# Kernel tuning notes

Measured on AMD Instinct MI355X. Metric: run time of the kernel, lower is better.

The kernel has to match this reference:

```python
import jax, jax.numpy as jnp
import numpy as np

N, T, D, H = 256, 64, 1024, 1024


def setup_inputs() -> dict:
    key = jax.random.key(0)
    k1, k2, k3, k4, k5 = jax.random.split(key, 5)
    x = jax.random.normal(k1, (N, T, D), dtype=jnp.float32)
    A = jax.random.normal(k2, (N, H, 4, 4), dtype=jnp.float32)
    Wx = jax.random.normal(k3, (D, 4 * H), dtype=jnp.float32) / np.sqrt(D)
    Wh = jax.random.normal(k4, (H, 4 * H), dtype=jnp.float32) / np.sqrt(H)
    Wattn = jax.random.normal(k5, (H, 4 * H), dtype=jnp.float32) / np.sqrt(H)
    b = jnp.zeros((4 * H,), dtype=jnp.float32)
    return {"x": x, "A": A, "Wx": Wx, "Wh": Wh, "Wattn": Wattn, "b": b}


def reference(x, A, Wx, Wh, Wattn, b):
    n, t, d = x.shape
    h_dim = A.shape[1]
    L = A.shape[2] * A.shape[3]  # 16 spatial locations
    A_flat = A.reshape(n, h_dim, L)  # (N, H, 16)
    scale = 1.0 / (h_dim ** 0.5)
    h0 = A_flat.mean(axis=2)  # global mean-pooled feature, (N, H)
    c0 = h0

    def step(carry, xt):
        h, c = carry
        # scaled dot-product attention over 4x4 grid
        w = jax.nn.softmax(jnp.einsum('nh,nhl->nl', h, A_flat) * scale, axis=1)
        attn = jnp.einsum('nhl,nl->nh', A_flat, w)
        a = h @ Wh + xt @ Wx + attn @ Wattn + b  # (N, 4H)
        a_i, a_f, a_o, a_g = jnp.split(a, 4, axis=1)
        i = jax.nn.sigmoid(a_i)
        f = jax.nn.sigmoid(a_f)
        o = jax.nn.sigmoid(a_o)
        g = jnp.tanh(a_g)
        c_next = f * c + i * g
        h_next = o * jnp.tanh(c_next)
        return (h_next, c_next), h_next

    xs = jnp.swapaxes(x, 0, 1)  # (T, N, D)
    _, hs = jax.lax.scan(step, (h0, c0), xs)
    return jnp.swapaxes(hs, 0, 1)  # (N, T, H)
```

## Files before the change

kernel.cpp:

```cpp
#include <hip/hip_runtime.h>
#include <math.h>

#define NB 256
#define TT 64
#define DD 1024
#define HH 1024

typedef __attribute__((ext_vector_type(8))) short short8;
typedef __attribute__((ext_vector_type(4))) float floatx4;

__device__ inline unsigned short f2bf(float f) {
    unsigned int u = __builtin_bit_cast(unsigned int, f);
    u += 0x7fffu + ((u >> 16) & 1u);
    return (unsigned short)(u >> 16);
}
__device__ inline float bf2f(unsigned int h16) {
    unsigned int u = h16 << 16;
    return __builtin_bit_cast(float, u);
}

__device__ inline void async_copy16(const unsigned short* g, unsigned short* l) {
    __builtin_amdgcn_global_load_lds(
        (const __attribute__((address_space(1))) unsigned int*)(g),
        (__attribute__((address_space(3))) unsigned int*)(l), 16, 0, 0);
}

__global__ void k_convW(const float* __restrict__ Wh,
                        const float* __restrict__ Wattn,
                        const float* __restrict__ Wx,
                        unsigned short* __restrict__ Wsw) {
    int u = blockIdx.x * 256 + threadIdx.x;
    int tile = u >> 9;
    int nj = tile / 48, kc = tile % 48;
    int within = u & 511;
    int kq = within >> 6, cc = within & 63;
    int k = kc * 64 + kq * 8;
    int col = (cc >> 4) * 1024 + nj * 16 + (cc & 15);
    const float* src;
    if (k < 1024)       src = Wh    + (size_t)k * 4096 + col;
    else if (k < 2048)  src = Wattn + (size_t)(k - 1024) * 4096 + col;
    else                src = Wx    + (size_t)(k - 2048) * 4096 + col;
    unsigned int w[4];
#pragma unroll
    for (int j = 0; j < 4; ++j) {
        unsigned int lo = f2bf(src[(size_t)(2 * j) * 4096]);
        unsigned int hi = f2bf(src[(size_t)(2 * j + 1) * 4096]);
        w[j] = lo | (hi << 16);
    }
    ((uint4*)Wsw)[u] = make_uint4(w[0], w[1], w[2], w[3]);
}

__global__ void k_convX(const float* __restrict__ x, unsigned short* __restrict__ xF) {
    int u = blockIdx.x * 256 + threadIdx.x;
    int t = u >> 15;
    int kq = (u >> 8) & 127;
    int m = u & 255;
    const float* src = x + (size_t)m * (TT * DD) + t * DD + kq * 8;
    float4 v0 = ((const float4*)src)[0];
    float4 v1 = ((const float4*)src)[1];
    unsigned int w0 = f2bf(v0.x) | (f2bf(v0.y) << 16);
    unsigned int w1 = f2bf(v0.z) | (f2bf(v0.w) << 16);
    unsigned int w2 = f2bf(v1.x) | (f2bf(v1.y) << 16);
    unsigned int w3 = f2bf(v1.z) | (f2bf(v1.w) << 16);
    ((uint4*)xF)[u] = make_uint4(w0, w1, w2, w3);
}

__global__ void k_convA_init(const float* __restrict__ A,
                             unsigned short* __restrict__ Abf,
                             float* __restrict__ h0,
                             float* __restrict__ c) {
    int idx = blockIdx.x * 256 + threadIdx.x;
    const float4* ap = (const float4*)(A + (size_t)idx * 16);
    float4 v0 = ap[0], v1 = ap[1], v2 = ap[2], v3 = ap[3];
    float vs[16] = {v0.x, v0.y, v0.z, v0.w, v1.x, v1.y, v1.z, v1.w,
                    v2.x, v2.y, v2.z, v2.w, v3.x, v3.y, v3.z, v3.w};
    float s = 0.f;
    unsigned int w[8];
#pragma unroll
    for (int j = 0; j < 8; ++j) {
        s += vs[2 * j] + vs[2 * j + 1];
        w[j] = f2bf(vs[2 * j]) | (f2bf(vs[2 * j + 1]) << 16);
    }
    ((uint4*)Abf)[idx * 2]     = make_uint4(w[0], w[1], w[2], w[3]);
    ((uint4*)Abf)[idx * 2 + 1] = make_uint4(w[4], w[5], w[6], w[7]);
    s *= (1.f / 16.f);
    h0[idx] = s;
    c[idx] = s;
}

__global__ __launch_bounds__(256) void k_attn(
    const unsigned short* __restrict__ Abf,
    const float* __restrict__ hprev, int hstride,
    unsigned short* __restrict__ lhsF) {
    const int n = blockIdx.x;
    const int tid = threadIdx.x;
    const int lane = tid & 63, wave = tid >> 6;

    float4 hv = *(const float4*)(hprev + (size_t)n * hstride + tid * 4);
    const uint4* ar = (const uint4*)(Abf + ((size_t)n * 1024 + tid * 4) * 16);

    float a[4][16];
#pragma unroll
    for (int r = 0; r < 4; ++r) {
        uint4 p0 = ar[r * 2], p1 = ar[r * 2 + 1];
        unsigned int ws[8] = {p0.x, p0.y, p0.z, p0.w, p1.x, p1.y, p1.z, p1.w};
#pragma unroll
        for (int j = 0; j < 8; ++j) {
            a[r][2 * j]     = bf2f(ws[j] & 0xffffu);
            a[r][2 * j + 1] = bf2f(ws[j] >> 16);
        }
    }
    float hvv[4] = {hv.x, hv.y, hv.z, hv.w};
    float s[16];
#pragma unroll
    for (int l = 0; l < 16; ++l) {
        float t = 0.f;
#pragma unroll
        for (int r = 0; r < 4; ++r) t += hvv[r] * a[r][l];
        s[l] = t;
    }

#pragma unroll
    for (int off = 32; off > 0; off >>= 1) {
#pragma unroll
        for (int l = 0; l < 16; ++l) s[l] += __shfl_xor(s[l], off, 64);
    }
    __shared__ float wred[4 * 16];
    if (lane == 0) {
#pragma unroll
        for (int l = 0; l < 16; ++l) wred[wave * 16 + l] = s[l];
    }
    __syncthreads();

    const float scale = 0.03125f;
    float sv[16];
#pragma unroll
    for (int l = 0; l < 16; ++l)
        sv[l] = (wred[l] + wred[16 + l] + wred[32 + l] + wred[48 + l]) * scale;
    float mx = sv[0];
#pragma unroll
    for (int l = 1; l < 16; ++l) mx = fmaxf(mx, sv[l]);
    float e[16], sum = 0.f;
#pragma unroll
    for (int l = 0; l < 16; ++l) { e[l] = __expf(sv[l] - mx); sum += e[l]; }
    float inv = 1.f / sum;
#pragma unroll
    for (int l = 0; l < 16; ++l) e[l] *= inv;

    unsigned short hb[4], ab[4];
#pragma unroll
    for (int r = 0; r < 4; ++r) {
        float acc = 0.f;
#pragma unroll
        for (int l = 0; l < 16; ++l) acc += a[r][l] * e[l];
        ab[r] = f2bf(acc);
        hb[r] = f2bf(hvv[r]);
    }
    unsigned int hw0 = (unsigned int)hb[0] | ((unsigned int)hb[1] << 16);
    unsigned int hw1 = (unsigned int)hb[2] | ((unsigned int)hb[3] << 16);
    unsigned int aw0 = (unsigned int)ab[0] | ((unsigned int)ab[1] << 16);
    unsigned int aw1 = (unsigned int)ab[2] | ((unsigned int)ab[3] << 16);
    size_t hu = ((size_t)(tid >> 1) * 256 + n) * 8 + (size_t)(tid & 1) * 4;
    size_t au = ((size_t)(128 + (tid >> 1)) * 256 + n) * 8 + (size_t)(tid & 1) * 4;
    *(uint2*)(lhsF + hu) = make_uint2(hw0, hw1);
    *(uint2*)(lhsF + au) = make_uint2(aw0, aw1);
}

__global__ __launch_bounds__(256) void k_step(
    const unsigned short* __restrict__ lhsF,
    const unsigned short* __restrict__ xFt,
    const unsigned short* __restrict__ Wsw,
    const float* __restrict__ b,
    float* __restrict__ c,
    float* __restrict__ out_t) {
    const int nj = blockIdx.x, mi = blockIdx.y;
    const int tid = threadIdx.x;
    const int lane = tid & 63, wave = tid >> 6;
    const int wm = wave & 1, wn = wave >> 1;
    const int l15 = lane & 15, quad = lane >> 4;
    const int waveBase = tid & ~63;

    __shared__ __align__(16) unsigned short lds[4 * 8192];

    floatx4 acc[2][2];
#pragma unroll
    for (int mt = 0; mt < 2; ++mt)
#pragma unroll
        for (int nt = 0; nt < 2; ++nt) acc[mt][nt] = (floatx4)0.f;

    const unsigned short* wTile = Wsw + (size_t)nj * (48 * 512 * 8);

    auto stage = [&](int kc, int buf) {
        unsigned short* la = lds + (size_t)buf * 8192;
        unsigned short* lb = la + 4096;
        const unsigned short* as_ = (kc < 32)
            ? lhsF + ((size_t)(kc * 8) * 256 + (size_t)mi * 64) * 8
            : xFt + ((size_t)((kc - 32) * 8) * 256 + (size_t)mi * 64) * 8;
#pragma unroll
        for (int i = 0; i < 2; ++i) {
            int idx = i * 256 + tid;
            int kq = idx >> 6, mm = idx & 63;
            async_copy16(as_ + ((size_t)kq * 256 + mm) * 8,
                         la + (size_t)(i * 256 + waveBase) * 8);
        }
        const unsigned short* bs = wTile + (size_t)kc * 512 * 8;
#pragma unroll
        for (int i = 0; i < 2; ++i) {
            int idx = i * 256 + tid;
            async_copy16(bs + (size_t)idx * 8,
                         lb + (size_t)(i * 256 + waveBase) * 8);
        }
    };

    auto compute = [&](int buf) {
        const unsigned short* la = lds + (size_t)buf * 8192;
        const unsigned short* lb = la + 4096;
#pragma unroll
        for (int ks = 0; ks < 2; ++ks) {
            const int kqq = ks * 4 + quad;
            short8 af[2], bfr[2];
#pragma unroll
            for (int mt = 0; mt < 2; ++mt)
                af[mt] = *(const short8*)(la + (size_t)(kqq * 64 + wm * 32 + mt * 16 + l15) * 8);
#pragma unroll
            for (int nt = 0; nt < 2; ++nt)
                bfr[nt] = *(const short8*)(lb + (size_t)(kqq * 64 + wn * 32 + nt * 16 + l15) * 8);
#pragma unroll
            for (int mt = 0; mt < 2; ++mt)
#pragma unroll
                for (int nt = 0; nt < 2; ++nt)
                    acc[mt][nt] = __builtin_amdgcn_mfma_f32_16x16x32_bf16(
                        af[mt], bfr[nt], acc[mt][nt], 0, 0, 0);
        }
    };

    stage(0, 0);
    stage(1, 1);
    stage(2, 2);

#pragma unroll 4
    for (int kc = 0; kc < 45; ++kc) {
        asm volatile("s_waitcnt vmcnt(8)\n\ts_barrier" ::: "memory");
        stage(kc + 3, (kc + 3) & 3);
        compute(kc & 3);
    }
    asm volatile("s_waitcnt vmcnt(8)\n\ts_barrier" ::: "memory");
    compute(45 & 3);
    asm volatile("s_waitcnt vmcnt(4)\n\ts_barrier" ::: "memory");
    compute(46 & 3);
    asm volatile("s_waitcnt vmcnt(0)\n\ts_barrier" ::: "memory");
    compute(47 & 3);

    __syncthreads();
    float* asF = (float*)lds;
#pragma unroll
    for (int mt = 0; mt < 2; ++mt)
#pragma unroll
        for (int nt = 0; nt < 2; ++nt)
#pragma unroll
            for (int r = 0; r < 4; ++r) {
                int row = wm * 32 + mt * 16 + quad * 4 + r;
                int cc = wn * 32 + nt * 16 + l15;
                asF[row * 64 + cc] = acc[mt][nt][r];
            }
    __syncthreads();

    const int j15 = tid & 15;
    const int jj = nj * 16 + j15;
    const float bi = b[jj], bf_ = b[1024 + jj], bo = b[2048 + jj], bg = b[3072 + jj];
#pragma unroll
    for (int i = 0; i < 4; ++i) {
        int cell = i * 256 + tid;
        int row = cell >> 4;
        float ai  = asF[row * 64 + j15]      + bi;
        float af2 = asF[row * 64 + 16 + j15] + bf_;
        float ao  = asF[row * 64 + 32 + j15] + bo;
        float ag  = asF[row * 64 + 48 + j15] + bg;
        float iv = 1.f / (1.f + __expf(-ai));
        float fv = 1.f / (1.f + __expf(-af2));
        float ov = 1.f / (1.f + __expf(-ao));
        float gv = 1.f - 2.f / (__expf(2.f * ag) + 1.f);
        int n = mi * 64 + row;
        size_t ci = (size_t)n * HH + jj;
        float cold = c[ci];
        float cn = fv * cold + iv * gv;
        c[ci] = cn;
        float th = 1.f - 2.f / (__expf(2.f * cn) + 1.f);
        out_t[(size_t)n * (TT * HH) + jj] = ov * th;
    }
}

extern "C" void kernel_launch(void* const* d_in, const int* in_sizes, int n_in,
                              void* d_out, int out_size, void* d_ws, size_t ws_size,
                              hipStream_t stream) {
    const float* x     = (const float*)d_in[0];
    const float* A     = (const float*)d_in[1];
    const float* Wx    = (const float*)d_in[2];
    const float* Wh    = (const float*)d_in[3];
    const float* Wattn = (const float*)d_in[4];
    const float* b     = (const float*)d_in[5];
    float* out = (float*)d_out;

    char* w = (char*)d_ws;
    unsigned short* Wsw  = (unsigned short*)(w);
    unsigned short* xF   = (unsigned short*)(w + 25165824);
    unsigned short* lhsF = (unsigned short*)(w + 58720256);
    unsigned short* Abf  = (unsigned short*)(w + 59768832);
    float* h0            = (float*)(w + 68157440);
    float* c             = (float*)(w + 69206016);

    k_convW<<<6144, 256, 0, stream>>>(Wh, Wattn, Wx, Wsw);
    k_convX<<<8192, 256, 0, stream>>>(x, xF);
    k_convA_init<<<1024, 256, 0, stream>>>(A, Abf, h0, c);

    for (int t = 0; t < TT; ++t) {
        const float* hprev = (t == 0) ? h0 : out + (size_t)(t - 1) * HH;
        int hstride = (t == 0) ? HH : TT * HH;
        k_attn<<<NB, 256, 0, stream>>>(Abf, hprev, hstride, lhsF);
        k_step<<<dim3(64, 4), 256, 0, stream>>>(
            lhsF, xF + (size_t)t * 262144, Wsw, b, c, out + (size_t)t * HH);
    }
}
```

Baseline: 1.351 ms.

## Split-K across waves with direct register loads in LSTM step GEMM

The step GEMM no longer stages A and B tiles through LDS with async copies and barriers. Each of the four waves instead computes the full 64x64 output tile over its own quarter of K (12 chunks), loading fragments straight from global memory into registers with double buffering. The partial sums are then reduced through shared memory in the gate epilogue. The x conversion kernel is also rewritten to transpose through LDS so that global reads and writes are coalesced. In exchange, register pressure rises (16 accumulators plus 32 fragment registers), the reduction needs 64KB of LDS, and operands are read from global memory without reuse across waves.

```diff
diff --git a/kernel.cpp b/kernel.cpp
--- a/kernel.cpp
+++ b/kernel.cpp
@@ -17,12 +17,6 @@
 __device__ inline float bf2f(unsigned int h16) {
     unsigned int u = h16 << 16;
     return __builtin_bit_cast(float, u);
-}
-
-__device__ inline void async_copy16(const unsigned short* g, unsigned short* l) {
-    __builtin_amdgcn_global_load_lds(
-        (const __attribute__((address_space(1))) unsigned int*)(g),
-        (__attribute__((address_space(3))) unsigned int*)(l), 16, 0, 0);
 }
 
 __global__ void k_convW(const float* __restrict__ Wh,
@@ -50,19 +44,32 @@
     ((uint4*)Wsw)[u] = make_uint4(w[0], w[1], w[2], w[3]);
 }
 
-__global__ void k_convX(const float* __restrict__ x, unsigned short* __restrict__ xF) {
-    int u = blockIdx.x * 256 + threadIdx.x;
-    int t = u >> 15;
-    int kq = (u >> 8) & 127;
-    int m = u & 255;
-    const float* src = x + (size_t)m * (TT * DD) + t * DD + kq * 8;
-    float4 v0 = ((const float4*)src)[0];
-    float4 v1 = ((const float4*)src)[1];
-    unsigned int w0 = f2bf(v0.x) | (f2bf(v0.y) << 16);
-    unsigned int w1 = f2bf(v0.z) | (f2bf(v0.w) << 16);
-    unsigned int w2 = f2bf(v1.x) | (f2bf(v1.y) << 16);
-    unsigned int w3 = f2bf(v1.z) | (f2bf(v1.w) << 16);
-    ((uint4*)xF)[u] = make_uint4(w0, w1, w2, w3);
+__global__ __launch_bounds__(256) void k_convX(const float* __restrict__ x,
+                                               unsigned short* __restrict__ xF) {
+    const int t  = blockIdx.x >> 4;
+    const int mb = blockIdx.x & 15;
+    const int tid = threadIdx.x;
+    __shared__ unsigned short xb[16][1032];
+
+#pragma unroll
+    for (int mm = 0; mm < 16; ++mm) {
+        int m = mb * 16 + mm;
+        const float4* src = (const float4*)(x + (size_t)m * (TT * DD) + (size_t)t * DD);
+        float4 v = src[tid];
+        unsigned int w0 = f2bf(v.x) | (f2bf(v.y) << 16);
+        unsigned int w1 = f2bf(v.z) | (f2bf(v.w) << 16);
+        *(uint2*)&xb[mm][tid * 4] = make_uint2(w0, w1);
+    }
+    __syncthreads();
+
+#pragma unroll
+    for (int i = 0; i < 8; ++i) {
+        int u = i * 256 + tid;
+        int kq = u >> 4, mm = u & 15;
+        uint4 val = *(const uint4*)&xb[mm][kq * 8];
+        size_t gu = (size_t)t * 32768 + (size_t)kq * 256 + mb * 16 + mm;
+        ((uint4*)xF)[gu] = val;
+    }
 }
 
 __global__ void k_convA_init(const float* __restrict__ A,
@@ -176,92 +183,71 @@
     const int nj = blockIdx.x, mi = blockIdx.y;
     const int tid = threadIdx.x;
     const int lane = tid & 63, wave = tid >> 6;
-    const int wm = wave & 1, wn = wave >> 1;
     const int l15 = lane & 15, quad = lane >> 4;
-    const int waveBase = tid & ~63;
-
-    __shared__ __align__(16) unsigned short lds[4 * 8192];
-
-    floatx4 acc[2][2];
-#pragma unroll
-    for (int mt = 0; mt < 2; ++mt)
-#pragma unroll
-        for (int nt = 0; nt < 2; ++nt) acc[mt][nt] = (floatx4)0.f;
+
+    floatx4 acc[4][4];
+#pragma unroll
+    for (int mt = 0; mt < 4; ++mt)
+#pragma unroll
+        for (int nt = 0; nt < 4; ++nt) acc[mt][nt] = (floatx4)0.f;
 
     const unsigned short* wTile = Wsw + (size_t)nj * (48 * 512 * 8);
 
-    auto stage = [&](int kc, int buf) {
-        unsigned short* la = lds + (size_t)buf * 8192;
-        unsigned short* lb = la + 4096;
-        const unsigned short* as_ = (kc < 32)
+    auto aBase = [&](int kc) -> const unsigned short* {
+        return (kc < 32)
             ? lhsF + ((size_t)(kc * 8) * 256 + (size_t)mi * 64) * 8
             : xFt + ((size_t)((kc - 32) * 8) * 256 + (size_t)mi * 64) * 8;
-#pragma unroll
-        for (int i = 0; i < 2; ++i) {
-            int idx = i * 256 + tid;
-            int kq = idx >> 6, mm = idx & 63;
-            async_copy16(as_ + ((size_t)kq * 256 + mm) * 8,
-                         la + (size_t)(i * 256 + waveBase) * 8);
-        }
-        const unsigned short* bs = wTile + (size_t)kc * 512 * 8;
-#pragma unroll
-        for (int i = 0; i < 2; ++i) {
-            int idx = i * 256 + tid;
-            async_copy16(bs + (size_t)idx * 8,
-                         lb + (size_t)(i * 256 + waveBase) * 8);
-        }
     };
 
-    auto compute = [&](int buf) {
-        const unsigned short* la = lds + (size_t)buf * 8192;
-        const unsigned short* lb = la + 4096;
-#pragma unroll
-        for (int ks = 0; ks < 2; ++ks) {
-            const int kqq = ks * 4 + quad;
-            short8 af[2], bfr[2];
-#pragma unroll
-            for (int mt = 0; mt < 2; ++mt)
-                af[mt] = *(const short8*)(la + (size_t)(kqq * 64 + wm * 32 + mt * 16 + l15) * 8);
-#pragma unroll
-            for (int nt = 0; nt < 2; ++nt)
-                bfr[nt] = *(const short8*)(lb + (size_t)(kqq * 64 + wn * 32 + nt * 16 + l15) * 8);
-#pragma unroll
-            for (int mt = 0; mt < 2; ++mt)
-#pragma unroll
-                for (int nt = 0; nt < 2; ++nt)
-                    acc[mt][nt] = __builtin_amdgcn_mfma_f32_16x16x32_bf16(
-                        af[mt], bfr[nt], acc[mt][nt], 0, 0, 0);
-        }
-    };
-
-    stage(0, 0);
-    stage(1, 1);
-    stage(2, 2);
-
-#pragma unroll 4
-    for (int kc = 0; kc < 45; ++kc) {
-        asm volatile("s_waitcnt vmcnt(8)\n\ts_barrier" ::: "memory");
-        stage(kc + 3, (kc + 3) & 3);
-        compute(kc & 3);
-    }
-    asm volatile("s_waitcnt vmcnt(8)\n\ts_barrier" ::: "memory");
-    compute(45 & 3);
-    asm volatile("s_waitcnt vmcnt(4)\n\ts_barrier" ::: "memory");
-    compute(46 & 3);
-    asm volatile("s_waitcnt vmcnt(0)\n\ts_barrier" ::: "memory");
-    compute(47 & 3);
-
-    __syncthreads();
-    float* asF = (float*)lds;
-#pragma unroll
-    for (int mt = 0; mt < 2; ++mt)
-#pragma unroll
-        for (int nt = 0; nt < 2; ++nt)
+    short8 A0[8], B0[8], A1[8], B1[8];
+
+#define LOADCH(Ar, Br, kc)                                                          \
+    do {                                                                            \
+        const unsigned short* ab_ = aBase(kc);                                      \
+        const unsigned short* bb_ = wTile + (size_t)(kc) * 4096;                    \
+        _Pragma("unroll") for (int mt = 0; mt < 4; ++mt)                            \
+            _Pragma("unroll") for (int ks = 0; ks < 2; ++ks)                        \
+                Ar[mt * 2 + ks] = *(const short8*)(ab_ +                            \
+                    (size_t)((ks * 4 + quad) * 256 + mt * 16 + l15) * 8);           \
+        _Pragma("unroll") for (int nt = 0; nt < 4; ++nt)                            \
+            _Pragma("unroll") for (int ks = 0; ks < 2; ++ks)                        \
+                Br[nt * 2 + ks] = *(const short8*)(bb_ +                            \
+                    (size_t)((ks * 4 + quad) * 64 + nt * 16 + l15) * 8);            \
+    } while (0)
+
+#define MMAC(Ar, Br)                                                                \
+    do {                                                                            \
+        _Pragma("unroll") for (int mt = 0; mt < 4; ++mt)                            \
+            _Pragma("unroll") for (int nt = 0; nt < 4; ++nt) {                      \
+                acc[mt][nt] = __builtin_amdgcn_mfma_f32_16x16x32_bf16(              \
+                    Ar[mt * 2 + 0], Br[nt * 2 + 0], acc[mt][nt], 0, 0, 0);          \
+                acc[mt][nt] = __builtin_amdgcn_mfma_f32_16x16x32_bf16(              \
+                    Ar[mt * 2 + 1], Br[nt * 2 + 1], acc[mt][nt], 0, 0, 0);          \
+            }                                                                       \
+    } while (0)
+
+    const int kc0 = wave * 12;
+    LOADCH(A0, B0, kc0);
+#pragma unroll
+    for (int i = 0; i < 6; ++i) {
+        LOADCH(A1, B1, kc0 + 2 * i + 1);
+        MMAC(A0, B0);
+        if (i < 5) LOADCH(A0, B0, kc0 + 2 * i + 2);
+        MMAC(A1, B1);
+    }
+#undef LOADCH
+#undef MMAC
+
+    __shared__ float red[4][4096];
+#pragma unroll
+    for (int mt = 0; mt < 4; ++mt)
+#pragma unroll
+        for (int nt = 0; nt < 4; ++nt)
 #pragma unroll
             for (int r = 0; r < 4; ++r) {
-                int row = wm * 32 + mt * 16 + quad * 4 + r;
-                int cc = wn * 32 + nt * 16 + l15;
-                asF[row * 64 + cc] = acc[mt][nt][r];
+                int row = mt * 16 + quad * 4 + r;
+                int cc = nt * 16 + l15;
+                red[wave][row * 64 + cc] = acc[mt][nt][r];
             }
     __syncthreads();
 
@@ -272,10 +258,14 @@
     for (int i = 0; i < 4; ++i) {
         int cell = i * 256 + tid;
         int row = cell >> 4;
-        float ai  = asF[row * 64 + j15]      + bi;
-        float af2 = asF[row * 64 + 16 + j15] + bf_;
-        float ao  = asF[row * 64 + 32 + j15] + bo;
-        float ag  = asF[row * 64 + 48 + j15] + bg;
+        float ai = bi, af2 = bf_, ao = bo, ag = bg;
+#pragma unroll
+        for (int w = 0; w < 4; ++w) {
+            ai  += red[w][row * 64 + j15];
+            af2 += red[w][row * 64 + 16 + j15];
+            ao  += red[w][row * 64 + 32 + j15];
+            ag  += red[w][row * 64 + 48 + j15];
+        }
         float iv = 1.f / (1.f + __expf(-ai));
         float fv = 1.f / (1.f + __expf(-af2));
         float ov = 1.f / (1.f + __expf(-ao));
@@ -310,7 +300,7 @@
     float* c             = (float*)(w + 69206016);
 
     k_convW<<<6144, 256, 0, stream>>>(Wh, Wattn, Wx, Wsw);
-    k_convX<<<8192, 256, 0, stream>>>(x, xF);
+    k_convX<<<1024, 256, 0, stream>>>(x, xF);
     k_convA_init<<<1024, 256, 0, stream>>>(A, Abf, h0, c);
 
     for (int t = 0; t < TT; ++t) {
```

Result: slower. 1.759 ms (+30.2%).

## Deepen k_step LDS prefetch pipeline to 8 buffers and coalesce convX via LDS transpose

Applied to the files above, without the earlier changes.

The per-step GEMM kernel now keeps six K-chunks in flight across eight LDS buffers instead of three across four. The vmcnt waits and the epilogue drain are adjusted to match. This is meant to hide more global-load latency in the weight-streaming GEMM, at the cost of doubling LDS use to 128 KB per block, which may reduce occupancy. Separately, the x-to-bf16 conversion now does fully coalesced row reads, stages the data in shared memory, then writes out the interleaved layout, replacing the earlier strided 32-byte reads.

```diff
diff --git a/kernel.cpp b/kernel.cpp
--- a/kernel.cpp
+++ b/kernel.cpp
@@ -50,19 +50,32 @@
     ((uint4*)Wsw)[u] = make_uint4(w[0], w[1], w[2], w[3]);
 }
 
-__global__ void k_convX(const float* __restrict__ x, unsigned short* __restrict__ xF) {
-    int u = blockIdx.x * 256 + threadIdx.x;
-    int t = u >> 15;
-    int kq = (u >> 8) & 127;
-    int m = u & 255;
-    const float* src = x + (size_t)m * (TT * DD) + t * DD + kq * 8;
-    float4 v0 = ((const float4*)src)[0];
-    float4 v1 = ((const float4*)src)[1];
-    unsigned int w0 = f2bf(v0.x) | (f2bf(v0.y) << 16);
-    unsigned int w1 = f2bf(v0.z) | (f2bf(v0.w) << 16);
-    unsigned int w2 = f2bf(v1.x) | (f2bf(v1.y) << 16);
-    unsigned int w3 = f2bf(v1.z) | (f2bf(v1.w) << 16);
-    ((uint4*)xF)[u] = make_uint4(w0, w1, w2, w3);
+__global__ __launch_bounds__(256) void k_convX(const float* __restrict__ x,
+                                               unsigned short* __restrict__ xF) {
+    const int t  = blockIdx.x >> 4;
+    const int mb = blockIdx.x & 15;
+    const int tid = threadIdx.x;
+    __shared__ unsigned short xb[16][1032];
+
+#pragma unroll
+    for (int mm = 0; mm < 16; ++mm) {
+        int m = mb * 16 + mm;
+        const float4* src = (const float4*)(x + (size_t)m * (TT * DD) + (size_t)t * DD);
+        float4 v = src[tid];
+        unsigned int w0 = f2bf(v.x) | (f2bf(v.y) << 16);
+        unsigned int w1 = f2bf(v.z) | (f2bf(v.w) << 16);
+        *(uint2*)&xb[mm][tid * 4] = make_uint2(w0, w1);
+    }
+    __syncthreads();
+
+#pragma unroll
+    for (int i = 0; i < 8; ++i) {
+        int u = i * 256 + tid;
+        int kq = u >> 4, mm = u & 15;
+        uint4 val = *(const uint4*)&xb[mm][kq * 8];
+        size_t gu = (size_t)t * 32768 + (size_t)kq * 256 + mb * 16 + mm;
+        ((uint4*)xF)[gu] = val;
+    }
 }
 
 __global__ void k_convA_init(const float* __restrict__ A,
@@ -180,7 +193,7 @@
     const int l15 = lane & 15, quad = lane >> 4;
     const int waveBase = tid & ~63;
 
-    __shared__ __align__(16) unsigned short lds[4 * 8192];
+    __shared__ __align__(16) unsigned short lds[8 * 8192];
 
     floatx4 acc[2][2];
 #pragma unroll
@@ -237,19 +250,28 @@
     stage(0, 0);
     stage(1, 1);
     stage(2, 2);
+    stage(3, 3);
+    stage(4, 4);
+    stage(5, 5);
 
 #pragma unroll 4
-    for (int kc = 0; kc < 45; ++kc) {
-        asm volatile("s_waitcnt vmcnt(8)\n\ts_barrier" ::: "memory");
-        stage(kc + 3, (kc + 3) & 3);
-        compute(kc & 3);
-    }
+    for (int kc = 0; kc < 42; ++kc) {
+        asm volatile("s_waitcnt vmcnt(20)\n\ts_barrier" ::: "memory");
+        stage(kc + 6, (kc + 6) & 7);
+        compute(kc & 7);
+    }
+    asm volatile("s_waitcnt vmcnt(20)\n\ts_barrier" ::: "memory");
+    compute(42 & 7);
+    asm volatile("s_waitcnt vmcnt(16)\n\ts_barrier" ::: "memory");
+    compute(43 & 7);
+    asm volatile("s_waitcnt vmcnt(12)\n\ts_barrier" ::: "memory");
+    compute(44 & 7);
     asm volatile("s_waitcnt vmcnt(8)\n\ts_barrier" ::: "memory");
-    compute(45 & 3);
+    compute(45 & 7);
     asm volatile("s_waitcnt vmcnt(4)\n\ts_barrier" ::: "memory");
-    compute(46 & 3);
+    compute(46 & 7);
     asm volatile("s_waitcnt vmcnt(0)\n\ts_barrier" ::: "memory");
-    compute(47 & 3);
+    compute(47 & 7);
 
     __syncthreads();
     float* asF = (float*)lds;
@@ -310,7 +332,7 @@
     float* c             = (float*)(w + 69206016);
 
     k_convW<<<6144, 256, 0, stream>>>(Wh, Wattn, Wx, Wsw);
-    k_convX<<<8192, 256, 0, stream>>>(x, xF);
+    k_convX<<<1024, 256, 0, stream>>>(x, xF);
     k_convA_init<<<1024, 256, 0, stream>>>(A, Abf, h0, c);
 
     for (int t = 0; t < TT; ++t) {
```

Measured after the change: 1.370 ms. No clear change (+1.4%).
